# Kernel optimization log

Hardware: AMD Instinct MI355X
Metric: run time of the kernel (lower is better)

Reference implementation:

```python
import jax, jax.numpy as jnp
import numpy as np

NBIN = 25
DELTA = 2.0 / (NBIN - 1)
EPS_COS = 1e-8   # torch CosineSimilarity eps
EPS_P = 1e-16    # pNumerator init in original


def setup_inputs() -> dict:
    key = jax.random.key(0)
    k1, k2, k3 = jax.random.split(key, 3)
    B, N, M = 16, 50000, 128
    qX = jax.random.normal(k1, (B, M), dtype=jnp.float32)
    dXs = jax.random.normal(k2, (B, N, M), dtype=jnp.float32)
    labels = jax.random.randint(k3, (B, N), 0, 2, dtype=jnp.int32)
    return {"qX": qX, "dXs": dXs, "labels": labels}


def _qap(qX, dXs, labels_f):
    # cosine similarity, matching torch.nn.CosineSimilarity (norms clamped at eps)
    num = jnp.einsum("bm,bnm->bn", qX, dXs)                      # (B, N)
    qn = jnp.maximum(jnp.linalg.norm(qX, axis=-1), EPS_COS)      # (B,)
    dn = jnp.maximum(jnp.linalg.norm(dXs, axis=-1), EPS_COS)     # (B, N)
    sim = num / (qn[:, None] * dn)                               # (B, N)

    # soft assignment to NBIN triangular bins centered at 1 - m*DELTA
    centers = 1.0 - jnp.arange(NBIN, dtype=sim.dtype) * DELTA    # (NBIN,)
    sa = jnp.clip(1.0 - jnp.abs(sim[..., None] - centers) / DELTA, 0.0)  # (B, N, NBIN)

    # per-bin reductions (computed once), then cumulative sums replace the O(nBin^2) loop
    num_per_bin = jnp.einsum("bnk,bn->bk", sa, labels_f)         # dot(sa[:,n], labels)
    den_per_bin = jnp.sum(sa, axis=1)                            # dot(sa[:,n], ones)

    pDen = jnp.cumsum(num_per_bin, axis=1)                       # (B, NBIN)
    pNum = EPS_P + jnp.cumsum(den_per_bin, axis=1)
    precision = pDen / pNum
    recall = num_per_bin / jnp.sum(labels_f, axis=1, keepdims=True)

    ap = jnp.sum(precision * recall, axis=1)                     # (B,)
    return jnp.mean(ap)


def reference(qX, dXs, labels):
    labels_f = labels.astype(qX.dtype)
    return _qap(qX, dXs, labels_f)
```

## Files before the change

### kernel.cpp

```cpp
#include <hip/hip_runtime.h>
#include <math.h>

#define NBIN 25
#define T 256
#define PAD 27
#define CHUNKS 64


__global__ __launch_bounds__(256)
void qap_accum(const float* __restrict__ qX, const float* __restrict__ dXs,
               const int* __restrict__ labels, float* __restrict__ ws, int N) {
    __shared__ float q[128];
    __shared__ float accN[T * PAD];
    __shared__ float accD[T * PAD];
    __shared__ float part[4 * 64];

    const int tid   = threadIdx.x;
    const int b     = blockIdx.x / CHUNKS;
    const int chunk = blockIdx.x % CHUNKS;

    if (tid < 128) q[tid] = qX[b * 128 + tid];
    for (int i = tid; i < T * PAD; i += T) { accN[i] = 0.f; accD[i] = 0.f; }
    __syncthreads();

    float qs = 0.f;
    #pragma unroll 8
    for (int j = 0; j < 128; ++j) qs = fmaf(q[j], q[j], qs);
    const float qn = fmaxf(sqrtf(qs), 1e-8f);

    const int per = (N + CHUNKS - 1) / CHUNKS;
    const int n0 = chunk * per;
    const int n1 = (n0 + per < N) ? (n0 + per) : N;

    const float4* q4 = reinterpret_cast<const float4*>(q);
    const int base = tid * PAD;
    float labCnt = 0.f;

    for (int n = n0 + tid; n < n1; n += T) {
        const float4* row =
            reinterpret_cast<const float4*>(dXs + ((size_t)b * N + n) * 128);
        float dot = 0.f, nrm = 0.f;
        #pragma unroll
        for (int j = 0; j < 32; ++j) {
            float4 x  = row[j];
            float4 qv = q4[j];
            dot = fmaf(x.x, qv.x, dot); dot = fmaf(x.y, qv.y, dot);
            dot = fmaf(x.z, qv.z, dot); dot = fmaf(x.w, qv.w, dot);
            nrm = fmaf(x.x, x.x, nrm);  nrm = fmaf(x.y, x.y, nrm);
            nrm = fmaf(x.z, x.z, nrm);  nrm = fmaf(x.w, x.w, nrm);
        }
        const float dn  = fmaxf(sqrtf(nrm), 1e-8f);
        const float sim = dot / (qn * dn);
        float p = (1.0f - sim) * 12.0f;
        p = fminf(fmaxf(p, 0.0f), 24.0f);
        int m = (int)p;
        if (m > 24) m = 24;
        const float frac = p - (float)m;
        const float lab  = (float)labels[(size_t)b * N + n];
        labCnt += lab;
        const float w0 = 1.0f - frac;
        accD[base + m] += w0;
        accN[base + m] += lab * w0;
        if (m + 1 < NBIN) {
            accD[base + m + 1] += frac;
            accN[base + m + 1] += lab * frac;
        }
    }
    accD[base + 25] = labCnt;
    __syncthreads();

    const int c  = tid & 63;
    const int qd = tid >> 6;
    if (c < 51) {
        const int idx = (c < 25) ? c : ((c < 50) ? (c - 25) : 25);
        const float* arr = (c < 25) ? accN : accD;
        float s = 0.f;
        const int t0 = qd * 64;
        #pragma unroll 8
        for (int t = t0; t < t0 + 64; ++t) s += arr[t * PAD + idx];
        part[qd * 64 + c] = s;
    }
    __syncthreads();
    if (tid < 51) {
        const float s = part[tid] + part[64 + tid] + part[128 + tid] + part[192 + tid];
        atomicAdd(&ws[b * 64 + tid], s);
    }
}

__global__ void qap_final(const float* __restrict__ ws, float* __restrict__ out, int B) {
    const int lane = threadIdx.x;
    float ap = 0.f;
    if (lane < B) {
        const float* w = ws + lane * 64;
        const float labSum = w[50];
        float cn = 0.f, cd = 0.f;
        for (int k = 0; k < NBIN; ++k) {
            const float nk = w[k];
            const float dk = w[25 + k];
            cn += nk;
            cd += dk;
            const float prec = cn / (1e-16f + cd);
            const float rec  = nk / labSum;
            ap = fmaf(prec, rec, ap);
        }
    }
    for (int off = 32; off > 0; off >>= 1) ap += __shfl_down(ap, off);
    if (lane == 0) out[0] = ap / (float)B;
}

extern "C" void kernel_launch(void* const* d_in, const int* in_sizes, int n_in,
                              void* d_out, int out_size, void* d_ws, size_t ws_size,
                              hipStream_t stream) {
    const float* qX     = (const float*)d_in[0];
    const float* dXs    = (const float*)d_in[1];
    const int*   labels = (const int*)d_in[2];
    float* out = (float*)d_out;
    float* ws  = (float*)d_ws;

    const int M = in_sizes[1] / in_sizes[2];
    const int B = in_sizes[0] / M;
    const int N = in_sizes[2] / B;
    (void)M;

    hipMemsetAsync(ws, 0, (size_t)B * 64 * sizeof(float), stream);
    qap_accum<<<B * CHUNKS, T, 0, stream>>>(qX, dXs, labels, ws, N);
    qap_final<<<1, 64, 0, stream>>>(ws, out, B);
}
```

Measured before the change: 544.4 us.

## Cooperative half-wave row loads with shuffle reductions and smaller chunks

```diff
diff --git a/kernel.cpp b/kernel.cpp
--- a/kernel.cpp
+++ b/kernel.cpp
@@ -4,87 +4,100 @@
 #define NBIN 25
 #define T 256
 #define PAD 27
-#define CHUNKS 64
+#define ROWS_PER_CHUNK 384
+#define ACC_ROWS 64
 
 
-__global__ __launch_bounds__(256)
+__global__ __launch_bounds__(256, 8)
 void qap_accum(const float* __restrict__ qX, const float* __restrict__ dXs,
-               const int* __restrict__ labels, float* __restrict__ ws, int N) {
-    __shared__ float q[128];
-    __shared__ float accN[T * PAD];
-    __shared__ float accD[T * PAD];
+               const int* __restrict__ labels, float* __restrict__ ws,
+               int N, int nChunks) {
+    __shared__ float accN[ACC_ROWS * PAD];
+    __shared__ float accD[ACC_ROWS * PAD];
+    __shared__ float labLds[ROWS_PER_CHUNK];
     __shared__ float part[4 * 64];
 
-    const int tid   = threadIdx.x;
-    const int b     = blockIdx.x / CHUNKS;
-    const int chunk = blockIdx.x % CHUNKS;
+    const int tid  = threadIdx.x;
+    const int b    = blockIdx.x / nChunks;
+    const int chunk= blockIdx.x % nChunks;
+    const int wave = tid >> 6;
+    const int lane = tid & 63;
+    const int half = lane >> 5;
+    const int sub  = lane & 31;
 
-    if (tid < 128) q[tid] = qX[b * 128 + tid];
-    for (int i = tid; i < T * PAD; i += T) { accN[i] = 0.f; accD[i] = 0.f; }
+    const int n0   = chunk * ROWS_PER_CHUNK;
+    const int n1   = min(n0 + ROWS_PER_CHUNK, N);
+    const int rows = n1 - n0;
+
+    for (int i = tid; i < ACC_ROWS * PAD; i += T) { accN[i] = 0.f; accD[i] = 0.f; }
+    for (int i = tid; i < rows; i += T)
+        labLds[i] = (float)labels[(size_t)b * N + n0 + i];
+
+    const float4 qv = reinterpret_cast<const float4*>(qX + b * 128)[sub];
+    float qs = qv.x*qv.x + qv.y*qv.y + qv.z*qv.z + qv.w*qv.w;
+    #pragma unroll
+    for (int mk = 1; mk <= 16; mk <<= 1) qs += __shfl_xor(qs, mk);
+    const float qn = fmaxf(sqrtf(qs), 1e-8f);
     __syncthreads();
 
-    float qs = 0.f;
-    #pragma unroll 8
-    for (int j = 0; j < 128; ++j) qs = fmaf(q[j], q[j], qs);
-    const float qn = fmaxf(sqrtf(qs), 1e-8f);
+    float labCnt = 0.f;
+    const int accRowBase = (wave << 4) + (half << 3);
+    const float* dbase = dXs + (size_t)b * N * 128;
 
-    const int per = (N + CHUNKS - 1) / CHUNKS;
-    const int n0 = chunk * per;
-    const int n1 = (n0 + per < N) ? (n0 + per) : N;
+    int r = n0 + (wave << 1) + half;
+    bool act = r < n1;
+    float4 x = make_float4(0.f, 0.f, 0.f, 0.f);
+    if (act) x = reinterpret_cast<const float4*>(dbase + (size_t)r * 128)[sub];
 
-    const float4* q4 = reinterpret_cast<const float4*>(q);
-    const int base = tid * PAD;
-    float labCnt = 0.f;
+    int it = 0;
+    while (act) {
+        const int rn = r + 8;
+        const bool actn = rn < n1;
+        float4 xn = make_float4(0.f, 0.f, 0.f, 0.f);
+        if (actn) xn = reinterpret_cast<const float4*>(dbase + (size_t)rn * 128)[sub];
 
-    for (int n = n0 + tid; n < n1; n += T) {
-        const float4* row =
-            reinterpret_cast<const float4*>(dXs + ((size_t)b * N + n) * 128);
-        float dot = 0.f, nrm = 0.f;
+        float dot = x.x*qv.x + x.y*qv.y + x.z*qv.z + x.w*qv.w;
+        float nr  = x.x*x.x  + x.y*x.y  + x.z*x.z  + x.w*x.w;
         #pragma unroll
-        for (int j = 0; j < 32; ++j) {
-            float4 x  = row[j];
-            float4 qv = q4[j];
-            dot = fmaf(x.x, qv.x, dot); dot = fmaf(x.y, qv.y, dot);
-            dot = fmaf(x.z, qv.z, dot); dot = fmaf(x.w, qv.w, dot);
-            nrm = fmaf(x.x, x.x, nrm);  nrm = fmaf(x.y, x.y, nrm);
-            nrm = fmaf(x.z, x.z, nrm);  nrm = fmaf(x.w, x.w, nrm);
+        for (int mk = 1; mk <= 16; mk <<= 1) {
+            dot += __shfl_xor(dot, mk);
+            nr  += __shfl_xor(nr,  mk);
         }
-        const float dn  = fmaxf(sqrtf(nrm), 1e-8f);
-        const float sim = dot / (qn * dn);
-        float p = (1.0f - sim) * 12.0f;
-        p = fminf(fmaxf(p, 0.0f), 24.0f);
-        int m = (int)p;
-        if (m > 24) m = 24;
-        const float frac = p - (float)m;
-        const float lab  = (float)labels[(size_t)b * N + n];
-        labCnt += lab;
-        const float w0 = 1.0f - frac;
-        accD[base + m] += w0;
-        accN[base + m] += lab * w0;
-        if (m + 1 < NBIN) {
-            accD[base + m + 1] += frac;
-            accN[base + m + 1] += lab * frac;
+        if (sub == (it & 7)) {
+            const float dn  = fmaxf(sqrtf(nr), 1e-8f);
+            const float sim = dot / (qn * dn);
+            float p = fminf(fmaxf((1.f - sim) * 12.f, 0.f), 24.f);
+            int m = (int)p; if (m > 24) m = 24;
+            const float frac = p - (float)m;
+            const float lab  = labLds[r - n0];
+            labCnt += lab;
+            const float w0 = 1.f - frac;
+            const int ba = (accRowBase + sub) * PAD;
+            accD[ba + m] += w0;
+            accN[ba + m] += lab * w0;
+            if (m + 1 < NBIN) {
+                accD[ba + m + 1] += frac;
+                accN[ba + m + 1] += lab * frac;
+            }
         }
+        r = rn; act = actn; x = xn; ++it;
     }
-    accD[base + 25] = labCnt;
+    if (sub < 8) accD[(accRowBase + sub) * PAD + 25] = labCnt;
     __syncthreads();
 
-    const int c  = tid & 63;
-    const int qd = tid >> 6;
+    const int c = tid & 63, g = tid >> 6;
     if (c < 51) {
         const int idx = (c < 25) ? c : ((c < 50) ? (c - 25) : 25);
         const float* arr = (c < 25) ? accN : accD;
         float s = 0.f;
-        const int t0 = qd * 64;
-        #pragma unroll 8
-        for (int t = t0; t < t0 + 64; ++t) s += arr[t * PAD + idx];
-        part[qd * 64 + c] = s;
+        #pragma unroll
+        for (int t = g * 16; t < g * 16 + 16; ++t) s += arr[t * PAD + idx];
+        part[g * 64 + c] = s;
     }
     __syncthreads();
-    if (tid < 51) {
-        const float s = part[tid] + part[64 + tid] + part[128 + tid] + part[192 + tid];
-        atomicAdd(&ws[b * 64 + tid], s);
-    }
+    if (tid < 51)
+        atomicAdd(&ws[b * 64 + tid],
+                  part[tid] + part[64 + tid] + part[128 + tid] + part[192 + tid]);
 }
 
 __global__ void qap_final(const float* __restrict__ ws, float* __restrict__ out, int B) {
@@ -122,7 +135,9 @@
     const int N = in_sizes[2] / B;
     (void)M;
 
+    const int nChunks = (N + ROWS_PER_CHUNK - 1) / ROWS_PER_CHUNK;
+
     hipMemsetAsync(ws, 0, (size_t)B * 64 * sizeof(float), stream);
-    qap_accum<<<B * CHUNKS, T, 0, stream>>>(qX, dXs, labels, ws, N);
+    qap_accum<<<B * nChunks, T, 0, stream>>>(qX, dXs, labels, ws, N, nChunks);
     qap_final<<<1, 64, 0, stream>>>(ws, out, B);
 }
```

Measured after the change: 579.9 us. 6.5% more time.
